# Performance work log

Hardware: AMD Instinct MI355X
Metric: run time of the kernel (lower is better)

Reference implementation:

```python
import jax, jax.numpy as jnp
import numpy as np
import math

B, T, C, H = 4, 2048, 1024, 16

def setup_inputs() -> dict:
    key = jax.random.key(0)
    ks = jax.random.split(key, 7)
    s = 0.02
    return {
        'x':  jax.random.normal(ks[0], (B, T, C), dtype=jnp.float32),
        'Wq': jax.random.normal(ks[1], (C, C), dtype=jnp.float32) * s,
        'bq': jnp.zeros((C,), dtype=jnp.float32),
        'Wk': jax.random.normal(ks[2], (C, C), dtype=jnp.float32) * s,
        'bk': jnp.zeros((C,), dtype=jnp.float32),
        'Wv': jax.random.normal(ks[3], (C, C), dtype=jnp.float32) * s,
        'bv': jnp.zeros((C,), dtype=jnp.float32),
    }

def reference(x, Wq, bq, Wk, bk, Wv, bv):
    # Dropouts are identity (eval mode). Note: the original module reuses
    # v_proj as the output projection -- reproduced faithfully.
    b, t, c = x.shape
    hs = c // H
    q = (x @ Wq + bq).reshape(b, t, H, hs).transpose(0, 2, 1, 3)  # [B,H,T,hs]
    k = (x @ Wk + bk).reshape(b, t, H, hs).transpose(0, 2, 1, 3)
    v = (x @ Wv + bv).reshape(b, t, H, hs).transpose(0, 2, 1, 3)
    att = jnp.einsum('bhqd,bhkd->bhqk', q, k) * (1.0 / math.sqrt(hs))
    causal = jnp.tril(jnp.ones((t, t), dtype=bool))
    att = jnp.where(causal[None, None], att, -jnp.inf)
    att = jax.nn.softmax(att, axis=-1)
    y = jnp.einsum('bhqk,bhkd->bhqd', att, v)  # [B,H,T,hs]
    y = y.transpose(0, 2, 1, 3).reshape(b, t, c)
    y = y @ Wv + bv  # module applies v_proj again as output projection
    return y
```

## Files before the change

### kernel.cpp

```cpp
#include <hip/hip_runtime.h>
#include <hip/hip_bf16.h>

typedef __bf16 bf16;
typedef __attribute__((ext_vector_type(8))) __bf16 bf16x8;
typedef __attribute__((ext_vector_type(4))) __bf16 bf16x4;
typedef __attribute__((ext_vector_type(2))) __bf16 bf16x2;
typedef __attribute__((ext_vector_type(4))) float f32x4;
typedef __attribute__((ext_vector_type(2))) unsigned int u32x2;
typedef __attribute__((ext_vector_type(4))) unsigned int u32x4;

#define MFMA16(a, b, c) __builtin_amdgcn_mfma_f32_16x16x32_bf16((a), (b), (c), 0, 0, 0)
#define SM_SCALE 0.18033688011112043f

__device__ __forceinline__ void gld_lds16(const bf16* g, bf16* l) {
    __builtin_amdgcn_global_load_lds((const __attribute__((address_space(1))) void*)g,
                                     (__attribute__((address_space(3))) void*)l, 16, 0, 0);
}

#define PBAR() asm volatile("s_barrier" ::: "memory")
#define VWAIT0() asm volatile("s_waitcnt vmcnt(0)" ::: "memory")
#define VWAIT3() asm volatile("s_waitcnt vmcnt(3)" ::: "memory")
#define VWAIT4() asm volatile("s_waitcnt vmcnt(4)" ::: "memory")

__global__ __launch_bounds__(256) void prep(const float* __restrict__ W0,
                                            const float* __restrict__ W1,
                                            const float* __restrict__ W2,
                                            bf16* __restrict__ Wt,
                                            const float* __restrict__ xin,
                                            bf16* __restrict__ xout) {
    __shared__ float tile[64][65];
    const int blk = blockIdx.x;
    const int tid = threadIdx.x;
    if (blk < 768) {
        const int z = blk >> 8, rem = blk & 255;
        const int r0 = (rem >> 4) * 64;
        const int c0 = (rem & 15) * 64;
        const float* W = (z == 0) ? W0 : ((z == 1) ? W1 : W2);
        bf16* dst = Wt + (size_t)z * 1024 * 1024;
        for (int i = tid; i < 4096; i += 256) {
            int r = i >> 6, cc = i & 63;
            tile[r][cc] = W[(size_t)(r0 + r) * 1024 + c0 + cc];
        }
        __syncthreads();
        for (int i = tid; i < 4096; i += 256) {
            int n = i >> 6, k = i & 63;
            dst[(size_t)(c0 + n) * 1024 + r0 + k] = (bf16)tile[k][n];
        }
    } else {
        const size_t i0 = ((size_t)(blk - 768) * 256 + tid) * 16;
#pragma unroll
        for (int j = 0; j < 2; j++) {
            const float4 v0 = *(const float4*)(xin + i0 + j * 8);
            const float4 v1 = *(const float4*)(xin + i0 + j * 8 + 4);
            bf16x8 o = {(bf16)v0.x, (bf16)v0.y, (bf16)v0.z, (bf16)v0.w,
                        (bf16)v1.x, (bf16)v1.y, (bf16)v1.z, (bf16)v1.w};
            *(bf16x8*)(xout + i0 + j * 8) = o;
        }
    }
}

template <int MODE>
__global__ __launch_bounds__(512, 4) void gemm_main(const bf16* __restrict__ A,
                                                    const bf16* __restrict__ Bt,
                                                    const float* __restrict__ b0,
                                                    const float* __restrict__ b1,
                                                    const float* __restrict__ b2,
                                                    void* __restrict__ out0,
                                                    void* __restrict__ out1,
                                                    void* __restrict__ out2,
                                                    int nbx) {
    __shared__ alignas(16) bf16 LDS[3 * 12288];

    const int orig = blockIdx.x;
    const int chunk = (int)gridDim.x >> 3;
    const int swz = (orig & 7) * chunk + (orig >> 3);
    const int by = swz / nbx, bx = swz % nbx;
    const int m0 = by * 256, n0 = bx * 128;

    const int tid = threadIdx.x;
    const int wid = tid >> 6, lane = tid & 63;
    const int wr = wid >> 1, wc = wid & 1;
    const int quad = lane >> 4, l16 = lane & 15;

    const int sr = tid >> 2;
    const int scol = (((tid & 3) ^ (sr & 3)) * 8);
    const bf16* gA = A + (size_t)(m0 + sr) * 1024 + scol;
    const bf16* gB = Bt + (size_t)(n0 + sr) * 1024 + scol;
    bf16* lA = &LDS[tid * 8];
    bf16* lB = &LDS[8192 + tid * 8];

    const int coff = ((quad ^ (l16 & 3)) * 8);

    f32x4 acc[4][4] = {};

    auto STAGE = [&](int kt, int p) {
        const int base = p * 12288;
        gld_lds16(gA + kt * 32, lA + base);
        gld_lds16(gA + kt * 32 + (size_t)128 * 1024, lA + base + 4096);
        gld_lds16(gB + kt * 32, lB + base);
    };

    STAGE(0, 0);
    STAGE(1, 1);
    VWAIT3();
    PBAR();

    int rb = 0;
    int sb = 2;
#pragma unroll 1
    for (int kt = 0; kt < 32; kt++) {
        const bf16* Asp = &LDS[rb * 12288];
        const bf16* Bsp = Asp + 8192;
        if (kt + 2 < 32) STAGE(kt + 2, sb);

        bf16x8 af[4], bfr[4];
#pragma unroll
        for (int m4 = 0; m4 < 4; m4++)
            af[m4] = *(const bf16x8*)&Asp[(wr * 64 + m4 * 16 + l16) * 32 + coff];
#pragma unroll
        for (int ni = 0; ni < 4; ni++)
            bfr[ni] = *(const bf16x8*)&Bsp[(wc * 64 + ni * 16 + l16) * 32 + coff];

        __builtin_amdgcn_s_setprio(1);
#pragma unroll
        for (int m4 = 0; m4 < 4; m4++)
#pragma unroll
            for (int ni = 0; ni < 4; ni++)
                acc[m4][ni] = MFMA16(af[m4], bfr[ni], acc[m4][ni]);
        __builtin_amdgcn_s_setprio(0);

        if (kt < 30) {
            VWAIT3();
            PBAR();
        } else if (kt == 30) {
            VWAIT0();
            PBAR();
        }
        rb = (rb == 2) ? 0 : rb + 1;
        sb = (sb == 2) ? 0 : sb + 1;
    }

    const int nl0 = (n0 & 1023) + wc * 64;
    const int mb0 = m0 + wr * 64;
    if (MODE == 0) {
        const int sel = n0 >> 10;
        if (sel < 2) {
            const float* bias = (sel == 0) ? b0 : b1;
            bf16* Cp = (bf16*)((sel == 0) ? out0 : out1);
            const float qs = (sel == 0) ? SM_SCALE : 1.0f;
#pragma unroll
            for (int mi = 0; mi < 4; mi++) {
                const int mbase = mb0 + mi * 16 + quad * 4;
#pragma unroll
                for (int ni = 0; ni < 4; ni++) {
                    const int nl = nl0 + ni * 16 + l16;
                    const float bv = bias[nl];
#pragma unroll
                    for (int r = 0; r < 4; r++)
                        Cp[(size_t)(mbase + r) * 1024 + nl] =
                            (bf16)((acc[mi][ni][r] + bv) * qs);
                }
            }
        } else {
            bf16* Vt = (bf16*)out2;
            const int b = m0 >> 11;
#pragma unroll
            for (int ni = 0; ni < 4; ni++) {
                const int nl = nl0 + ni * 16 + l16;
                const int h = nl >> 6, d = nl & 63;
                const float bv = b2[nl];
                bf16* dst = Vt + ((size_t)(b * 16 + h) * 64 + d) * 2048;
#pragma unroll
                for (int mi = 0; mi < 4; mi++) {
                    const int t0 = (mb0 + mi * 16 + quad * 4) & 2047;
                    bf16x4 w = {(bf16)(acc[mi][ni][0] + bv), (bf16)(acc[mi][ni][1] + bv),
                                (bf16)(acc[mi][ni][2] + bv), (bf16)(acc[mi][ni][3] + bv)};
                    *(bf16x4*)&dst[t0] = w;
                }
            }
        }
    } else {
        float* Cp = (float*)out0;
#pragma unroll
        for (int mi = 0; mi < 4; mi++) {
            const int mbase = mb0 + mi * 16 + quad * 4;
#pragma unroll
            for (int ni = 0; ni < 4; ni++) {
                const int n = n0 + wc * 64 + ni * 16 + l16;
                const float bv = b0[n];
#pragma unroll
                for (int r = 0; r < 4; r++)
                    Cp[(size_t)(mbase + r) * 1024 + n] = acc[mi][ni][r] + bv;
            }
        }
    }
}

template <bool NEEDMASK>
__device__ __forceinline__ void softmax_reg(const f32x4* st, bf16x8* pf, int qrel) {
    unsigned int p[4][2];
#pragma unroll
    for (int j = 0; j < 4; j++) {
        float pv[4];
#pragma unroll
        for (int r = 0; r < 4; r++) {
            float s = st[j][r];
            if (NEEDMASK && (j * 16 + r > qrel)) s = -1e30f;
            pv[r] = __builtin_amdgcn_exp2f(s);
        }
        bf16x2 w0 = {(bf16)pv[0], (bf16)pv[1]};
        bf16x2 w1 = {(bf16)pv[2], (bf16)pv[3]};
        p[j][0] = __builtin_bit_cast(unsigned int, w0);
        p[j][1] = __builtin_bit_cast(unsigned int, w1);
    }
#pragma unroll
    for (int ks = 0; ks < 2; ks++) {
        unsigned int q4[4];
#pragma unroll
        for (int h = 0; h < 2; h++) {
            u32x2 s32 = __builtin_amdgcn_permlane32_swap(p[2 * ks][h], p[2 * ks + 1][h],
                                                         false, false);
            u32x2 s16 = __builtin_amdgcn_permlane16_swap(s32[0], s32[1], false, false);
            q4[h] = s16[0];
            q4[2 + h] = s16[1];
        }
        u32x4 qq = {q4[0], q4[1], q4[2], q4[3]};
        pf[ks] = __builtin_bit_cast(bf16x8, qq);
    }
}

__global__ __launch_bounds__(256, 3) void attn(const bf16* __restrict__ Q,
                                               const bf16* __restrict__ Kg,
                                               const bf16* __restrict__ Vt,
                                               bf16* __restrict__ O) {
    const int lin = blockIdx.y * 16 + blockIdx.x;
    const int bh = (lin & 7) * 8 + ((lin >> 3) & 7);
    const int jb = lin >> 6;
    const int b = bh >> 4, h = bh & 15;
    const int tid = threadIdx.x;
    const int wave = tid >> 6, lane = tid & 63;
    const int quad = lane >> 4, l16 = lane & 15;

    __shared__ alignas(16) bf16 KVs[3 * 8192];

    const bf16* Kbase = Kg + ((size_t)b * 2048) * 1024 + h * 64;
    const bf16* Vbase = Vt + (size_t)bh * 64 * 2048;

    const int srow = tid >> 3;
    const int schunk = (tid & 7) ^ (srow & 7);

    const int xorE = (l16 & 7) * 8;
    const int cofA = (quad * 8) ^ xorE;
    const int cofB = (32 + quad * 8) ^ xorE;

    const bf16 one1 = (bf16)1.0f;
    const bf16x8 onesf = {one1, one1, one1, one1, one1, one1, one1, one1};

#pragma unroll 1
    for (int phase = 0; phase < 2; phase++) {
        const int qs = (phase == 0) ? (31 - jb) : jb;
        const int q0 = qs * 64;
        const bf16* Qbase = Q + ((size_t)(b * 2048 + q0)) * 1024 + h * 64;

        bf16x8 qf[2];
#pragma unroll
        for (int ks = 0; ks < 2; ks++)
            qf[ks] = *(const bf16x8*)&Qbase[(size_t)(wave * 16 + l16) * 1024 + ks * 32 + quad * 8];

        f32x4 ot[4] = {};
        f32x4 lacc = {0.f, 0.f, 0.f, 0.f};
        const int ntiles = qs + 1;
        const int qrel = wave * 16 + l16 - quad * 4;

        const bf16* pK = Kbase + (size_t)srow * 1024 + schunk * 8;
        const bf16* pK2 = pK + (size_t)32 * 1024;
        const bf16* pV = Vbase + (size_t)srow * 2048 + schunk * 8;
        const bf16* pV2 = pV + (size_t)32 * 2048;

        {
            bf16* nb = &KVs[tid * 8];
            gld_lds16(pK, nb);
            gld_lds16(pK2, nb + 2048);
            gld_lds16(pV, nb + 4096);
            gld_lds16(pV2, nb + 6144);
            pK += 64 * 1024; pK2 += 64 * 1024; pV += 64; pV2 += 64;
            nb = &KVs[8192 + tid * 8];
            gld_lds16(pK, nb);
            gld_lds16(pK2, nb + 2048);
            gld_lds16(pV, nb + 4096);
            gld_lds16(pV2, nb + 6144);
            pK += 64 * 1024; pK2 += 64 * 1024; pV += 64; pV2 += 64;
        }
        VWAIT4();
        PBAR();

        int rbuf = 0, sbuf = 2;
#pragma unroll 1
        for (int tk = 0; tk < ntiles; tk++) {
            const bf16* buf = &KVs[rbuf * 8192];
            if (tk + 2 < ntiles) {
                bf16* nb = &KVs[sbuf * 8192 + tid * 8];
                gld_lds16(pK, nb);
                gld_lds16(pK2, nb + 2048);
                gld_lds16(pV, nb + 4096);
                gld_lds16(pV2, nb + 6144);
                pK += 64 * 1024; pK2 += 64 * 1024; pV += 64; pV2 += 64;
            }

            f32x4 st[4] = {};
#pragma unroll
            for (int ks = 0; ks < 2; ks++)
#pragma unroll
                for (int j = 0; j < 4; j++) {
                    const bf16x8 kf =
                        *(const bf16x8*)&buf[(j * 16 + l16) * 64 + (ks ? cofB : cofA)];
                    st[j] = MFMA16(kf, qf[ks], st[j]);
                }

            bf16x8 pf[2];
            if (tk == ntiles - 1)
                softmax_reg<true>(st, pf, qrel);
            else
                softmax_reg<false>(st, pf, qrel);

            lacc = MFMA16(onesf, pf[0], lacc);
            lacc = MFMA16(onesf, pf[1], lacc);

#pragma unroll
            for (int ks = 0; ks < 2; ks++)
#pragma unroll
                for (int db = 0; db < 4; db++) {
                    const bf16x8 vf = *(const bf16x8*)&buf[4096 + (db * 16 + l16) * 64 +
                                                           (ks ? cofB : cofA)];
                    ot[db] = MFMA16(vf, pf[ks], ot[db]);
                }

            if (tk + 1 < ntiles) {
                if (tk + 2 < ntiles) VWAIT4();
                else VWAIT0();
                PBAR();
            }
            rbuf = (rbuf == 2) ? 0 : rbuf + 1;
            sbuf = (sbuf == 2) ? 0 : sbuf + 1;
        }

        const float inv = 1.f / lacc[0];
        bf16* ep = &KVs[((ntiles + 1) % 3) * 8192 + wave * (16 * 72)];
#pragma unroll
        for (int db = 0; db < 4; db++) {
            bf16x4 w = {(bf16)(ot[db][0] * inv), (bf16)(ot[db][1] * inv),
                        (bf16)(ot[db][2] * inv), (bf16)(ot[db][3] * inv)};
            *(bf16x4*)&ep[l16 * 72 + db * 16 + quad * 4] = w;
        }
        {
            const int orow = lane >> 2, oc = (lane & 3) * 16;
            bf16* Obase =
                O + ((size_t)(b * 2048 + q0 + wave * 16 + orow)) * 1024 + h * 64 + oc;
            const bf16* src = &ep[orow * 72 + oc];
            *(bf16x8*)&Obase[0] = *(const bf16x8*)&src[0];
            *(bf16x8*)&Obase[8] = *(const bf16x8*)&src[8];
        }
        __syncthreads();
    }
}

extern "C" void kernel_launch(void* const* d_in, const int* in_sizes, int n_in,
                              void* d_out, int out_size, void* d_ws, size_t ws_size,
                              hipStream_t stream) {
    const float* x = (const float*)d_in[0];
    const float* Wq = (const float*)d_in[1];
    const float* bq = (const float*)d_in[2];
    const float* Wk = (const float*)d_in[3];
    const float* bk = (const float*)d_in[4];
    const float* Wv = (const float*)d_in[5];
    const float* bv = (const float*)d_in[6];
    float* out = (float*)d_out;

    const int M = 8192;
    const size_t sz_x = (size_t)M * 1024;
    const size_t sz_w = (size_t)1024 * 1024;

    char* p = (char*)d_ws;
    bf16* xb = (bf16*)p;   p += sz_x * 2;
    bf16* Wcat = (bf16*)p; p += 3 * sz_w * 2;
    bf16* qb = (bf16*)p;   p += sz_x * 2;
    bf16* kb = (bf16*)p;   p += sz_x * 2;
    bf16* Vt = (bf16*)p;   p += sz_x * 2;
    bf16* yatt = (bf16*)p; p += sz_x * 2;

    prep<<<dim3(2816), dim3(256), 0, stream>>>(Wq, Wk, Wv, Wcat, x, xb);

    gemm_main<0><<<dim3(768), dim3(512), 0, stream>>>(xb, Wcat, bq, bk, bv, qb, kb, Vt, 24);
    attn<<<dim3(16, 64), dim3(256), 0, stream>>>(qb, kb, Vt, yatt);
    gemm_main<1><<<dim3(256), dim3(512), 0, stream>>>(yatt, Wcat + 2 * sz_w, bv, bv, bv,
                                                      out, out, out, 8);
}
```

Before: 229.1 us.

## Process 128 query rows per attention block sharing K/V tiles; tweak GEMM LDS swizzle

Each attention block now computes two 64-row query groups against every K/V tile it stages in LDS. This halves K/V global-to-LDS traffic per query row and doubles the MFMA work per barrier. The grid shrinks to 512 one-dimensional blocks, still pairing the heavy and light causal chunks for balance. The trade-offs are more registers, occupancy bounds lowered from 3 to 2, and a fully masked extra tile computed for the first group. The GEMM's LDS XOR swizzle also changes to use (row>>1)&3, likely to cut bank conflicts on fragment reads.

```diff
diff --git a/kernel.cpp b/kernel.cpp
--- a/kernel.cpp
+++ b/kernel.cpp
@@ -83,13 +83,13 @@
     const int quad = lane >> 4, l16 = lane & 15;
 
     const int sr = tid >> 2;
-    const int scol = (((tid & 3) ^ (sr & 3)) * 8);
+    const int scol = (((tid & 3) ^ ((sr >> 1) & 3)) * 8);
     const bf16* gA = A + (size_t)(m0 + sr) * 1024 + scol;
     const bf16* gB = Bt + (size_t)(n0 + sr) * 1024 + scol;
     bf16* lA = &LDS[tid * 8];
     bf16* lB = &LDS[8192 + tid * 8];
 
-    const int coff = ((quad ^ (l16 & 3)) * 8);
+    const int coff = ((quad ^ ((l16 >> 1) & 3)) * 8);
 
     f32x4 acc[4][4] = {};
 
@@ -229,11 +229,11 @@
     }
 }
 
-__global__ __launch_bounds__(256, 3) void attn(const bf16* __restrict__ Q,
+__global__ __launch_bounds__(256, 2) void attn(const bf16* __restrict__ Q,
                                                const bf16* __restrict__ Kg,
                                                const bf16* __restrict__ Vt,
                                                bf16* __restrict__ O) {
-    const int lin = blockIdx.y * 16 + blockIdx.x;
+    const int lin = blockIdx.x;
     const int bh = (lin & 7) * 8 + ((lin >> 3) & 7);
     const int jb = lin >> 6;
     const int b = bh >> 4, h = bh & 15;
@@ -258,18 +258,20 @@
 
 #pragma unroll 1
     for (int phase = 0; phase < 2; phase++) {
-        const int qs = (phase == 0) ? (31 - jb) : jb;
-        const int q0 = qs * 64;
+        const int js = (phase == 0) ? (15 - jb) : jb;
+        const int q0 = js * 128;
         const bf16* Qbase = Q + ((size_t)(b * 2048 + q0)) * 1024 + h * 64;
 
-        bf16x8 qf[2];
-#pragma unroll
-        for (int ks = 0; ks < 2; ks++)
-            qf[ks] = *(const bf16x8*)&Qbase[(size_t)(wave * 16 + l16) * 1024 + ks * 32 + quad * 8];
-
-        f32x4 ot[4] = {};
-        f32x4 lacc = {0.f, 0.f, 0.f, 0.f};
-        const int ntiles = qs + 1;
+        bf16x8 qfA[2], qfB[2];
+#pragma unroll
+        for (int ks = 0; ks < 2; ks++) {
+            qfA[ks] = *(const bf16x8*)&Qbase[(size_t)(wave * 16 + l16) * 1024 + ks * 32 + quad * 8];
+            qfB[ks] = *(const bf16x8*)&Qbase[(size_t)(64 + wave * 16 + l16) * 1024 + ks * 32 + quad * 8];
+        }
+
+        f32x4 otA[4] = {}, otB[4] = {};
+        f32x4 laccA = {0.f, 0.f, 0.f, 0.f}, laccB = {0.f, 0.f, 0.f, 0.f};
+        const int ntiles = 2 * js + 2;
         const int qrel = wave * 16 + l16 - quad * 4;
 
         const bf16* pK = Kbase + (size_t)srow * 1024 + schunk * 8;
@@ -307,24 +309,33 @@
                 pK += 64 * 1024; pK2 += 64 * 1024; pV += 64; pV2 += 64;
             }
 
-            f32x4 st[4] = {};
+            f32x4 stA[4] = {}, stB[4] = {};
 #pragma unroll
             for (int ks = 0; ks < 2; ks++)
 #pragma unroll
                 for (int j = 0; j < 4; j++) {
                     const bf16x8 kf =
                         *(const bf16x8*)&buf[(j * 16 + l16) * 64 + (ks ? cofB : cofA)];
-                    st[j] = MFMA16(kf, qf[ks], st[j]);
+                    stA[j] = MFMA16(kf, qfA[ks], stA[j]);
+                    stB[j] = MFMA16(kf, qfB[ks], stB[j]);
                 }
 
-            bf16x8 pf[2];
-            if (tk == ntiles - 1)
-                softmax_reg<true>(st, pf, qrel);
-            else
-                softmax_reg<false>(st, pf, qrel);
-
-            lacc = MFMA16(onesf, pf[0], lacc);
-            lacc = MFMA16(onesf, pf[1], lacc);
+            bf16x8 pfA[2], pfB[2];
+            if (tk < ntiles - 2) {
+                softmax_reg<false>(stA, pfA, qrel);
+                softmax_reg<false>(stB, pfB, qrel);
+            } else if (tk == ntiles - 2) {
+                softmax_reg<true>(stA, pfA, qrel);
+                softmax_reg<false>(stB, pfB, qrel);
+            } else {
+                softmax_reg<true>(stA, pfA, qrel - 64);
+                softmax_reg<true>(stB, pfB, qrel);
+            }
+
+            laccA = MFMA16(onesf, pfA[0], laccA);
+            laccA = MFMA16(onesf, pfA[1], laccA);
+            laccB = MFMA16(onesf, pfB[0], laccB);
+            laccB = MFMA16(onesf, pfB[1], laccB);
 
 #pragma unroll
             for (int ks = 0; ks < 2; ks++)
@@ -332,7 +343,8 @@
                 for (int db = 0; db < 4; db++) {
                     const bf16x8 vf = *(const bf16x8*)&buf[4096 + (db * 16 + l16) * 64 +
                                                            (ks ? cofB : cofA)];
-                    ot[db] = MFMA16(vf, pf[ks], ot[db]);
+                    otA[db] = MFMA16(vf, pfA[ks], otA[db]);
+                    otB[db] = MFMA16(vf, pfB[ks], otB[db]);
                 }
 
             if (tk + 1 < ntiles) {
@@ -344,18 +356,32 @@
             sbuf = (sbuf == 2) ? 0 : sbuf + 1;
         }
 
-        const float inv = 1.f / lacc[0];
         bf16* ep = &KVs[((ntiles + 1) % 3) * 8192 + wave * (16 * 72)];
-#pragma unroll
-        for (int db = 0; db < 4; db++) {
-            bf16x4 w = {(bf16)(ot[db][0] * inv), (bf16)(ot[db][1] * inv),
-                        (bf16)(ot[db][2] * inv), (bf16)(ot[db][3] * inv)};
-            *(bf16x4*)&ep[l16 * 72 + db * 16 + quad * 4] = w;
-        }
+        const int orow = lane >> 2, oc = (lane & 3) * 16;
         {
-            const int orow = lane >> 2, oc = (lane & 3) * 16;
+            const float inv = 1.f / laccA[0];
+#pragma unroll
+            for (int db = 0; db < 4; db++) {
+                bf16x4 w = {(bf16)(otA[db][0] * inv), (bf16)(otA[db][1] * inv),
+                            (bf16)(otA[db][2] * inv), (bf16)(otA[db][3] * inv)};
+                *(bf16x4*)&ep[l16 * 72 + db * 16 + quad * 4] = w;
+            }
             bf16* Obase =
                 O + ((size_t)(b * 2048 + q0 + wave * 16 + orow)) * 1024 + h * 64 + oc;
+            const bf16* src = &ep[orow * 72 + oc];
+            *(bf16x8*)&Obase[0] = *(const bf16x8*)&src[0];
+            *(bf16x8*)&Obase[8] = *(const bf16x8*)&src[8];
+        }
+        {
+            const float inv = 1.f / laccB[0];
+#pragma unroll
+            for (int db = 0; db < 4; db++) {
+                bf16x4 w = {(bf16)(otB[db][0] * inv), (bf16)(otB[db][1] * inv),
+                            (bf16)(otB[db][2] * inv), (bf16)(otB[db][3] * inv)};
+                *(bf16x4*)&ep[l16 * 72 + db * 16 + quad * 4] = w;
+            }
+            bf16* Obase =
+                O + ((size_t)(b * 2048 + q0 + 64 + wave * 16 + orow)) * 1024 + h * 64 + oc;
             const bf16* src = &ep[orow * 72 + oc];
             *(bf16x8*)&Obase[0] = *(const bf16x8*)&src[0];
             *(bf16x8*)&Obase[8] = *(const bf16x8*)&src[8];
@@ -391,7 +417,7 @@
     prep<<<dim3(2816), dim3(256), 0, stream>>>(Wq, Wk, Wv, Wcat, x, xb);
 
     gemm_main<0><<<dim3(768), dim3(512), 0, stream>>>(xb, Wcat, bq, bk, bv, qb, kb, Vt, 24);
-    attn<<<dim3(16, 64), dim3(256), 0, stream>>>(qb, kb, Vt, yatt);
+    attn<<<dim3(512), dim3(256), 0, stream>>>(qb, kb, Vt, yatt);
     gemm_main<1><<<dim3(256), dim3(512), 0, stream>>>(yatt, Wcat + 2 * sz_w, bv, bv, bv,
                                                       out, out, out, 8);
 }
```

Result: no change. 228.1 us (-0.5%).
